# Kernel tuning notes

Measured on AMD Instinct MI355X. Metric: run time of the kernel, lower is better.

The kernel has to match this reference:

```python
import jax, jax.numpy as jnp
import numpy as np
import math

EMBED_DIM = 512
NUM_HEADS = 8
B, T = 1, 4096

def setup_inputs() -> dict:
    key = jax.random.key(0)
    ks = jax.random.split(key, 12)
    D = EMBED_DIM
    s = 1.0 / math.sqrt(D)
    inp = {
        "x": jax.random.normal(ks[0], (B, T, D), dtype=jnp.float32),
        "ln1_scale": jnp.ones((D,), jnp.float32),
        "ln1_bias": jnp.zeros((D,), jnp.float32),
        "Wq": jax.random.normal(ks[1], (D, D), jnp.float32) * s,
        "bq": jnp.zeros((D,), jnp.float32),
        "Wk": jax.random.normal(ks[2], (D, D), jnp.float32) * s,
        "bk": jnp.zeros((D,), jnp.float32),
        "Wv": jax.random.normal(ks[3], (D, D), jnp.float32) * s,
        "bv": jnp.zeros((D,), jnp.float32),
        "Wo": jax.random.normal(ks[4], (D, D), jnp.float32) * s,
        "bo": jnp.zeros((D,), jnp.float32),
        "ln2_scale": jnp.ones((D,), jnp.float32),
        "ln2_bias": jnp.zeros((D,), jnp.float32),
        "W1": jax.random.normal(ks[5], (D, 4 * D), jnp.float32) * s,
        "b1": jnp.zeros((4 * D,), jnp.float32),
        "W2": jax.random.normal(ks[6], (4 * D, D), jnp.float32) * (1.0 / math.sqrt(4 * D)),
        "b2": jnp.zeros((D,), jnp.float32),
    }
    return inp

def _layernorm(x, scale, bias, eps=1e-6):
    mu = jnp.mean(x, axis=-1, keepdims=True)
    var = jnp.mean(jnp.square(x - mu), axis=-1, keepdims=True)
    return (x - mu) * jax.lax.rsqrt(var + eps) * scale + bias

def reference(x, ln1_scale, ln1_bias, Wq, bq, Wk, bk, Wv, bv, Wo, bo,
              ln2_scale, ln2_bias, W1, b1, W2, b2):
    Bb, Tt, D = x.shape
    H = NUM_HEADS
    hd = D // H
    residual = x
    h = _layernorm(x, ln1_scale, ln1_bias)
    q = (h @ Wq + bq).reshape(Bb, Tt, H, hd).transpose(0, 2, 1, 3)
    k = (h @ Wk + bk).reshape(Bb, Tt, H, hd).transpose(0, 2, 1, 3)
    v = (h @ Wv + bv).reshape(Bb, Tt, H, hd).transpose(0, 2, 1, 3)
    # [B,H,T,T] scores (naive attention as in the original module)
    scores = jnp.einsum('bhqd,bhkd->bhqk', q, k) / math.sqrt(hd)
    probs = jax.nn.softmax(scores, axis=-1)
    out = jnp.einsum('bhqk,bhkd->bhqd', probs, v).transpose(0, 2, 1, 3).reshape(Bb, Tt, D)
    h = out @ Wo + bo  # dropout deterministic -> identity
    x = h + residual
    residual = x
    h = _layernorm(x, ln2_scale, ln2_bias)
    h = jax.nn.gelu(h @ W1 + b1, approximate=True)
    h = h @ W2 + b2
    return h + residual
```

## Files before the change

### kernel.cpp

```cpp
#include <hip/hip_runtime.h>
#include <hip/hip_bf16.h>
#include <stdint.h>

typedef __bf16 bf16;
typedef __bf16 bf16x4 __attribute__((ext_vector_type(4)));
typedef __bf16 bf16x8 __attribute__((ext_vector_type(8)));
typedef float  f32x4  __attribute__((ext_vector_type(4)));
typedef float  f32x16 __attribute__((ext_vector_type(16)));

#define MFMA32(A_, B_, C_) __builtin_amdgcn_mfma_f32_32x32x16_bf16((A_), (B_), (C_), 0, 0, 0)

#define QSCALE 0.1803368801111137f

__device__ __forceinline__ void gload_lds16(const void* g, void* l) {
  __builtin_amdgcn_global_load_lds(
      (const __attribute__((address_space(1))) unsigned int*)g,
      (__attribute__((address_space(3))) unsigned int*)l, 16, 0, 0);
}

__device__ __forceinline__ unsigned pk2(float lo, float hi_) {
  union { bf16 h[2]; unsigned u; } t;
  t.h[0] = (bf16)lo; t.h[1] = (bf16)hi_;
  return t.u;
}

__device__ __forceinline__ float fast_exp2(float x) {
#if __has_builtin(__builtin_amdgcn_exp2f)
  return __builtin_amdgcn_exp2f(x);
#else
  return exp2f(x);
#endif
}

__global__ __launch_bounds__(256) void prep_ln(const float* __restrict__ Wq,
                                               const float* __restrict__ Wk,
                                               const float* __restrict__ Wv,
                                               const float* __restrict__ Wo,
                                               const float* __restrict__ W1,
                                               const float* __restrict__ W2,
                                               const float* __restrict__ bq,
                                               const float* __restrict__ bk,
                                               const float* __restrict__ bv,
                                               bf16* __restrict__ wqkvT, bf16* __restrict__ woT,
                                               bf16* __restrict__ w1T, bf16* __restrict__ w2T,
                                               float* __restrict__ bqkv,
                                               const float* __restrict__ x,
                                               const float* __restrict__ ln1s,
                                               const float* __restrict__ ln1b,
                                               bf16* __restrict__ h) {
  const int b = blockIdx.x;
  if (b >= 774) {
    const int w = threadIdx.x >> 6, l = threadIdx.x & 63;
    const int row = (b - 774) * 4 + w;
    const float4* xp = (const float4*)(x + (size_t)row * 512 + l * 8);
    float4 v0 = xp[0], v1 = xp[1];
    float xv[8] = {v0.x, v0.y, v0.z, v0.w, v1.x, v1.y, v1.z, v1.w};
    float s = 0.f, q = 0.f;
#pragma unroll
    for (int j = 0; j < 8; ++j) { s += xv[j]; q += xv[j] * xv[j]; }
#pragma unroll
    for (int m = 1; m < 64; m <<= 1) { s += __shfl_xor(s, m); q += __shfl_xor(q, m); }
    const float mean = s * (1.f / 512.f);
    const float var = q * (1.f / 512.f) - mean * mean;
    const float rstd = rsqrtf(var + 1e-6f);
    const float4* scp = (const float4*)(ln1s + l * 8);
    const float4* bip = (const float4*)(ln1b + l * 8);
    float4 s0 = scp[0], s1 = scp[1], b0 = bip[0], b1 = bip[1];
    float sv[8] = {s0.x, s0.y, s0.z, s0.w, s1.x, s1.y, s1.z, s1.w};
    float bvv[8] = {b0.x, b0.y, b0.z, b0.w, b1.x, b1.y, b1.z, b1.w};
    bf16x8 ov;
#pragma unroll
    for (int j = 0; j < 8; ++j) ov[j] = (bf16)((xv[j] - mean) * rstd * sv[j] + bvv[j]);
    *(bf16x8*)(h + (size_t)row * 512 + l * 8) = ov;
    return;
  }
  if (b >= 768) {
    int i = (b - 768) * 256 + threadIdx.x;
    if (i < 1536)
      bqkv[i] = (i < 512) ? bq[i] * QSCALE : (i < 1024 ? bk[i - 512] : bv[i - 1024]);
    return;
  }
  const float* in; bf16* outp; int K, N, t; float sc = 1.f;
  if (b < 64)       { in = Wq; outp = wqkvT;              K = 512;  N = 512;  t = b;       sc = QSCALE; }
  else if (b < 128) { in = Wk; outp = wqkvT + 512 * 512;  K = 512;  N = 512;  t = b - 64;  }
  else if (b < 192) { in = Wv; outp = wqkvT + 1024 * 512; K = 512;  N = 512;  t = b - 128; }
  else if (b < 256) { in = Wo; outp = woT;                K = 512;  N = 512;  t = b - 192; }
  else if (b < 512) { in = W1; outp = w1T;                K = 512;  N = 2048; t = b - 256; }
  else              { in = W2; outp = w2T;                K = 2048; N = 512;  t = b - 512; }
  const int tx = K >> 6;
  const int k0 = (t % tx) * 64, n0 = (t / tx) * 64;
  __shared__ bf16 tile[64][72];
  const int tid = threadIdx.x;
#pragma unroll
  for (int s = 0; s < 16; ++s) {
    int j = tid + s * 256;
    int r = j >> 6, c = j & 63;
    tile[r][c] = (bf16)(in[(size_t)(k0 + r) * N + n0 + c] * sc);
  }
  __syncthreads();
#pragma unroll
  for (int s = 0; s < 16; ++s) {
    int j = tid + s * 256;
    int n = j >> 6, k = j & 63;
    outp[(size_t)(n0 + n) * K + k0 + k] = tile[k][n];
  }
}

__global__ __launch_bounds__(256) void ln_k(const float* __restrict__ x,
                                            const float* __restrict__ sc,
                                            const float* __restrict__ bi,
                                            bf16* __restrict__ out) {
  const int w = threadIdx.x >> 6, l = threadIdx.x & 63;
  const int row = blockIdx.x * 4 + w;
  const float4* xp = (const float4*)(x + (size_t)row * 512 + l * 8);
  float4 v0 = xp[0], v1 = xp[1];
  float xv[8] = {v0.x, v0.y, v0.z, v0.w, v1.x, v1.y, v1.z, v1.w};
  float s = 0.f, q = 0.f;
#pragma unroll
  for (int j = 0; j < 8; ++j) { s += xv[j]; q += xv[j] * xv[j]; }
#pragma unroll
  for (int m = 1; m < 64; m <<= 1) { s += __shfl_xor(s, m); q += __shfl_xor(q, m); }
  const float mean = s * (1.f / 512.f);
  const float var = q * (1.f / 512.f) - mean * mean;
  const float rstd = rsqrtf(var + 1e-6f);
  const float4* scp = (const float4*)(sc + l * 8);
  const float4* bip = (const float4*)(bi + l * 8);
  float4 s0 = scp[0], s1 = scp[1], b0 = bip[0], b1 = bip[1];
  float sv[8] = {s0.x, s0.y, s0.z, s0.w, s1.x, s1.y, s1.z, s1.w};
  float bvv[8] = {b0.x, b0.y, b0.z, b0.w, b1.x, b1.y, b1.z, b1.w};
  bf16x8 ov;
#pragma unroll
  for (int j = 0; j < 8; ++j) ov[j] = (bf16)((xv[j] - mean) * rstd * sv[j] + bvv[j]);
  *(bf16x8*)(out + (size_t)row * 512 + l * 8) = ov;
}

template <int EPI>
__global__ __launch_bounds__(256, 3) void gemm32(const bf16* __restrict__ A,
                                                 const bf16* __restrict__ Bt,
                                                 const float* __restrict__ bias,
                                                 const float* __restrict__ res,
                                                 void* __restrict__ outp,
                                                 int M, int N, int K) {
  __shared__ bf16 a_lds[3][64 * 64];
  __shared__ bf16 b_lds[3][64 * 64];
  const int m0 = blockIdx.x * 64, n0 = blockIdx.y * 64;
  const int tid = threadIdx.x, l = tid & 63, w = tid >> 6;
  const int wm = w >> 1, wn = w & 1;
  const int hi = l >> 5, l5 = l & 31;
  const int lr = l >> 3;
  const int cs = (l & 7) ^ (lr & 7);
  const int swl = l5 & 7;

  const bf16* ag = A + (size_t)(m0 + w * 16 + lr) * K + cs * 8;
  const bf16* bg = Bt + (size_t)(n0 + w * 16 + lr) * K + cs * 8;
  const size_t r8 = (size_t)8 * K;

#define GS32(B_)                                                   \
  do {                                                             \
    gload_lds16(ag,      (char*)a_lds[(B_)] + (w * 16) * 128);     \
    gload_lds16(ag + r8, (char*)a_lds[(B_)] + (w * 16 + 8) * 128); \
    gload_lds16(bg,      (char*)b_lds[(B_)] + (w * 16) * 128);     \
    gload_lds16(bg + r8, (char*)b_lds[(B_)] + (w * 16 + 8) * 128); \
    ag += 64; bg += 64;                                            \
  } while (0)

  f32x16 acc = {};
  const int kiters = K >> 6;
  GS32(0);
  GS32(1);
  asm volatile("s_waitcnt vmcnt(4)" ::: "memory");
  __builtin_amdgcn_s_barrier();
  for (int kt = 0; kt < kiters; ++kt) {
    if (kt + 2 < kiters) GS32((kt + 2) % 3);
    const bf16* ab = a_lds[kt % 3] + (wm * 32 + l5) * 64;
    const bf16* bb = b_lds[kt % 3] + (wn * 32 + l5) * 64;
#pragma unroll
    for (int kk = 0; kk < 4; ++kk) {
      bf16x8 af = *(const bf16x8*)(ab + ((kk * 2 + hi) ^ swl) * 8);
      bf16x8 bf_ = *(const bf16x8*)(bb + ((kk * 2 + hi) ^ swl) * 8);
      acc = MFMA32(bf_, af, acc);
    }
    if (kt + 1 < kiters) {
      if (kt + 2 < kiters) asm volatile("s_waitcnt vmcnt(4)" ::: "memory");
      else                 asm volatile("s_waitcnt vmcnt(0)" ::: "memory");
      __builtin_amdgcn_s_barrier();
    }
  }
#undef GS32

  const int row = m0 + wm * 32 + l5;
#pragma unroll
  for (int rg = 0; rg < 4; ++rg) {
    const int cb = n0 + wn * 32 + rg * 8 + hi * 4;
    float4 bb4 = *(const float4*)(bias + cb);
    float v[4];
    v[0] = acc[rg * 4 + 0] + bb4.x;
    v[1] = acc[rg * 4 + 1] + bb4.y;
    v[2] = acc[rg * 4 + 2] + bb4.z;
    v[3] = acc[rg * 4 + 3] + bb4.w;
    float4 rr = *(const float4*)(res + (size_t)row * N + cb);
    *(float4*)((float*)outp + (size_t)row * N + cb) =
        make_float4(v[0] + rr.x, v[1] + rr.y, v[2] + rr.z, v[3] + rr.w);
  }
}

template <int EPI>
__global__ __launch_bounds__(256, 3) void gemm_w(const bf16* __restrict__ A,
                                                 const bf16* __restrict__ Bt,
                                                 const float* __restrict__ bias,
                                                 void* __restrict__ outp,
                                                 bf16* __restrict__ k2,
                                                 bf16* __restrict__ v2,
                                                 int M, int N, int K) {
  __shared__ __align__(16) char smem[49152];
  char* a_lds = smem;
  char* b_lds = smem + 24576;
  const int tid = threadIdx.x, l = tid & 63, w = tid >> 6;
  const int wm = w >> 1, wn = w & 1;
  const int hi = l >> 5, l5 = l & 31;
  const int m0 = blockIdx.x * 128, n0 = blockIdx.y * 128;
  const int swl = l5 & 7;

  const int sr = tid >> 3, sp = tid & 7;
  const int slc = sp ^ (sr & 7);
  const int shalf = slc >> 2, skc = slc & 3;
  const bf16* ag = A + (size_t)(m0 + shalf * 64 + sr) * K + skc * 8;
  const bf16* bg = Bt + (size_t)(n0 + shalf * 64 + sr) * K + skc * 8;
  const size_t r32 = (size_t)32 * K;

#define GSW(B_)                                                       \
  do {                                                                \
    gload_lds16(ag,       a_lds + (B_) * 8192 + w * 1024);            \
    gload_lds16(ag + r32, a_lds + (B_) * 8192 + 4096 + w * 1024);     \
    gload_lds16(bg,       b_lds + (B_) * 8192 + w * 1024);            \
    gload_lds16(bg + r32, b_lds + (B_) * 8192 + 4096 + w * 1024);     \
    ag += 32; bg += 32;                                               \
  } while (0)

  f32x16 acc00 = {}, acc01 = {}, acc10 = {}, acc11 = {};
  const int kiters = K >> 5;
  GSW(0);
  GSW(1);
  asm volatile("s_waitcnt vmcnt(4)" ::: "memory");
  __builtin_amdgcn_s_barrier();
  for (int kt = 0; kt < kiters; ++kt) {
    if (kt + 2 < kiters) GSW((kt + 2) % 3);
    const char* ab = a_lds + (kt % 3) * 8192;
    const char* bb = b_lds + (kt % 3) * 8192;
#pragma unroll
    for (int kk = 0; kk < 2; ++kk) {
      bf16x8 af0 = *(const bf16x8*)(ab + (l5)*128      + ((wm * 4 + kk * 2 + hi) ^ swl) * 16);
      bf16x8 af1 = *(const bf16x8*)(ab + (32 + l5)*128 + ((wm * 4 + kk * 2 + hi) ^ swl) * 16);
      bf16x8 bf0 = *(const bf16x8*)(bb + (l5)*128      + ((wn * 4 + kk * 2 + hi) ^ swl) * 16);
      bf16x8 bf1 = *(const bf16x8*)(bb + (32 + l5)*128 + ((wn * 4 + kk * 2 + hi) ^ swl) * 16);
      acc00 = MFMA32(bf0, af0, acc00);
      acc01 = MFMA32(bf1, af0, acc01);
      acc10 = MFMA32(bf0, af1, acc10);
      acc11 = MFMA32(bf1, af1, acc11);
    }
    if (kt + 1 < kiters) {
      if (kt + 2 < kiters) asm volatile("s_waitcnt vmcnt(4)" ::: "memory");
      else                 asm volatile("s_waitcnt vmcnt(0)" ::: "memory");
      __builtin_amdgcn_s_barrier();
    }
  }
#undef GSW

  if constexpr (EPI == 2) {
#pragma unroll
    for (int mi = 0; mi < 2; ++mi) {
      const int row = m0 + wm * 64 + mi * 32 + l5;
#pragma unroll
      for (int ni = 0; ni < 2; ++ni) {
        const f32x16& ac = (mi == 0) ? (ni == 0 ? acc00 : acc01)
                                     : (ni == 0 ? acc10 : acc11);
#pragma unroll
        for (int rg = 0; rg < 4; ++rg) {
          const int cb = n0 + wn * 64 + ni * 32 + rg * 8 + hi * 4;
          float4 bb4 = *(const float4*)(bias + cb);
          float v[4] = {ac[rg * 4 + 0] + bb4.x, ac[rg * 4 + 1] + bb4.y,
                        ac[rg * 4 + 2] + bb4.z, ac[rg * 4 + 3] + bb4.w};
          bf16x4 o;
#pragma unroll
          for (int e = 0; e < 4; ++e) {
            float t = -2.3022077697f * (v[e] + 0.044715f * v[e] * v[e] * v[e]);
            o[e] = (bf16)(v[e] / (1.f + fast_exp2(t)));
          }
          *(bf16x4*)((bf16*)outp + (size_t)row * N + cb) = o;
        }
      }
    }
  } else {
    __syncthreads();
    bf16(*ct)[136] = (bf16(*)[136])smem;
#pragma unroll
    for (int mi = 0; mi < 2; ++mi) {
      const int rl = wm * 64 + mi * 32 + l5;
#pragma unroll
      for (int ni = 0; ni < 2; ++ni) {
        const f32x16& ac = (mi == 0) ? (ni == 0 ? acc00 : acc01)
                                     : (ni == 0 ? acc10 : acc11);
#pragma unroll
        for (int rg = 0; rg < 4; ++rg) {
          const int cl = wn * 64 + ni * 32 + rg * 8 + hi * 4;
          float4 bb4 = *(const float4*)(bias + n0 + cl);
          bf16x4 o;
          o[0] = (bf16)(ac[rg * 4 + 0] + bb4.x);
          o[1] = (bf16)(ac[rg * 4 + 1] + bb4.y);
          o[2] = (bf16)(ac[rg * 4 + 2] + bb4.z);
          o[3] = (bf16)(ac[rg * 4 + 3] + bb4.w);
          *(bf16x4*)(&ct[rl][cl]) = o;
        }
      }
    }
    __syncthreads();
    if (n0 < 512) {
#pragma unroll
      for (int p = 0; p < 8; ++p) {
        int v = p * 256 + tid;
        int r = v >> 4, c8 = (v & 15) * 8;
        *(bf16x8*)((bf16*)outp + (size_t)(m0 + r) * 512 + n0 + c8) =
            *(const bf16x8*)(&ct[r][c8]);
      }
    } else if (n0 < 1024) {
      const int hb = (n0 - 512) >> 6;
#pragma unroll
      for (int p = 0; p < 8; ++p) {
        int v = p * 256 + tid;
        int r = v >> 4, c8 = (v & 15) * 8;
        *(bf16x8*)(k2 + (size_t)(hb + (c8 >> 6)) * 262144 +
                   (size_t)(m0 + r) * 64 + (c8 & 63)) = *(const bf16x8*)(&ct[r][c8]);
      }
    } else {
      const int hb = (n0 - 1024) >> 6;
      const int d = tid >> 2, t8 = (tid & 3) * 8;
#pragma unroll
      for (int h2 = 0; h2 < 2; ++h2) {
        bf16* vb = v2 + (size_t)(hb + h2) * 262144 + (size_t)(m0 >> 5) * 2048;
#pragma unroll
        for (int p = 0; p < 4; ++p) {
          bf16x8 vv;
#pragma unroll
          for (int e = 0; e < 8; ++e) vv[e] = ct[p * 32 + t8 + e][h2 * 64 + d];
          *(bf16x8*)(vb + p * 2048 + d * 32 + t8) = vv;
        }
      }
    }
  }
}

__global__ __launch_bounds__(512, 4) void attn_k(const bf16* __restrict__ q2,
                                                 const bf16* __restrict__ k2,
                                                 const bf16* __restrict__ v2,
                                                 bf16* __restrict__ attnb) {
  const int bid = blockIdx.x;
  const int head = bid & 7;
  const int qt = bid >> 3;
  const int w = threadIdx.x >> 6, l = threadIdx.x & 63;
  const int hi = l >> 5, l5 = l & 31;
  const int pair = w >> 1, wq = w & 1;

  __shared__ __align__(16) char smem[65536];
  char* kt_l = smem + pair * 16384;
  char* vt_l = kt_l + 8192;

  const int qrow0 = qt * 64 + wq * 32;
  const bf16* qb = q2 + (size_t)(qrow0 + l5) * 512 + head * 64;
  bf16x8 qf[4];
#pragma unroll
  for (int cc = 0; cc < 4; ++cc) qf[cc] = *(const bf16x8*)(qb + cc * 16 + hi * 8);

  const int kstart = pair * 1024;

  const int lr = l >> 3;
  const int lc3 = (l & 7) ^ lr;
  const char* kg = (const char*)k2 + (size_t)head * 524288 + (size_t)kstart * 128 +
                   (wq * 16 + lr) * 128 + lc3 * 16;
  const char* vg = (const char*)v2 + (size_t)head * 524288 + (size_t)(kstart >> 5) * 4096 +
                   (lc3 >> 2) * 2048 + (wq * 16 + lr) * 64 + (lc3 & 3) * 16;
  const int kdst = wq * 2048;

#define STAGE(B_)                                                            \
  do {                                                                       \
    gload_lds16(kg,        kt_l + (B_) * 4096 + kdst);                       \
    gload_lds16(kg + 1024, kt_l + (B_) * 4096 + kdst + 1024);                \
    gload_lds16(vg,        vt_l + (B_) * 4096 + kdst);                       \
    gload_lds16(vg + 512,  vt_l + (B_) * 4096 + kdst + 1024);                \
    kg += 4096; vg += 4096;                                                  \
  } while (0)

  STAGE(0);
  __syncthreads();

  f32x16 o0 = {}, o1 = {};
  float psum = 0.f;
  const int swl = l5 & 7;
  const char* kbase = kt_l + l5 * 128;
  const char* vbase = vt_l + l5 * 128;

  for (int t = 0; t < 32; ++t) {
    const int cur = t & 1;
    if (t < 31) STAGE(cur ^ 1);

    __builtin_amdgcn_s_setprio(1);
    f32x16 s = {};
#pragma unroll
    for (int cc = 0; cc < 4; ++cc) {
      bf16x8 kf = *(const bf16x8*)(kbase + cur * 4096 + ((cc * 2 + hi) ^ swl) * 16);
      s = MFMA32(kf, qf[cc], s);
    }
    __builtin_amdgcn_s_setprio(0);

#pragma unroll
    for (int c = 0; c < 2; ++c) {
      float p[8];
#pragma unroll
      for (int j = 0; j < 8; ++j) p[j] = fast_exp2(s[c * 8 + j]);
      psum += ((p[0] + p[1]) + (p[2] + p[3])) + ((p[4] + p[5]) + (p[6] + p[7]));
      unsigned X = pk2(p[0], p[1]), X2 = pk2(p[2], p[3]);
      unsigned Y = pk2(p[4], p[5]), Y2 = pk2(p[6], p[7]);
      asm volatile("v_permlane32_swap_b32 %0, %1" : "+v"(X), "+v"(Y));
      asm volatile("v_permlane32_swap_b32 %0, %1" : "+v"(X2), "+v"(Y2));
      union { unsigned wd[4]; bf16x8 v; } pa;
      pa.wd[0] = X; pa.wd[1] = X2; pa.wd[2] = Y; pa.wd[3] = Y2;
      bf16x8 vf0 = *(const bf16x8*)(vbase + cur * 4096 + ((c * 2 + hi) ^ swl) * 16);
      bf16x8 vf1 = *(const bf16x8*)(vbase + cur * 4096 + ((4 + c * 2 + hi) ^ swl) * 16);
      __builtin_amdgcn_s_setprio(1);
      o0 = MFMA32(vf0, pa.v, o0);
      o1 = MFMA32(vf1, pa.v, o1);
      __builtin_amdgcn_s_setprio(0);
    }
    __syncthreads();
  }
#undef STAGE

  float* comb = (float*)smem;
  if (pair > 0) {
    float* cb = comb + (((pair - 1) * 2 + wq) * 64 + l) * 33;
#pragma unroll
    for (int r = 0; r < 16; ++r) { cb[r] = o0[r]; cb[16 + r] = o1[r]; }
    cb[32] = psum;
  }
  __syncthreads();
  if (pair == 0) {
#pragma unroll
    for (int p = 0; p < 3; ++p) {
      const float* cb = comb + ((p * 2 + wq) * 64 + l) * 33;
#pragma unroll
      for (int r = 0; r < 16; ++r) { o0[r] += cb[r]; o1[r] += cb[16 + r]; }
      psum += cb[32];
    }
    const float lsum = psum + __shfl_xor(psum, 32);
    const float inv = 1.f / lsum;
    bf16* ob = attnb + (size_t)(qrow0 + l5) * 512 + head * 64;
#pragma unroll
    for (int dt = 0; dt < 2; ++dt)
#pragma unroll
      for (int rg = 0; rg < 4; ++rg) {
        bf16x4 vv;
#pragma unroll
        for (int e = 0; e < 4; ++e) {
          const float ov = (dt == 0) ? o0[rg * 4 + e] : o1[rg * 4 + e];
          vv[e] = (bf16)(ov * inv);
        }
        *(bf16x4*)(ob + dt * 32 + rg * 8 + hi * 4) = vv;
      }
  }
}

extern "C" void kernel_launch(void* const* d_in, const int* in_sizes, int n_in,
                              void* d_out, int out_size, void* d_ws, size_t ws_size,
                              hipStream_t stream) {
  const float* x    = (const float*)d_in[0];
  const float* ln1s = (const float*)d_in[1];
  const float* ln1b = (const float*)d_in[2];
  const float* Wq   = (const float*)d_in[3];
  const float* bq   = (const float*)d_in[4];
  const float* Wk   = (const float*)d_in[5];
  const float* bk   = (const float*)d_in[6];
  const float* Wv   = (const float*)d_in[7];
  const float* bv   = (const float*)d_in[8];
  const float* Wo   = (const float*)d_in[9];
  const float* bo   = (const float*)d_in[10];
  const float* ln2s = (const float*)d_in[11];
  const float* ln2b = (const float*)d_in[12];
  const float* W1   = (const float*)d_in[13];
  const float* b1   = (const float*)d_in[14];
  const float* W2   = (const float*)d_in[15];
  const float* b2   = (const float*)d_in[16];
  float* out = (float*)d_out;

  char* ws = (char*)d_ws;
  bf16*  wqkvT = (bf16*)(ws + 0);
  bf16*  woT   = (bf16*)(ws + 1572864);
  bf16*  w1T   = (bf16*)(ws + 2097152);
  bf16*  w2T   = (bf16*)(ws + 4194304);
  float* bqkv  = (float*)(ws + 6291456);
  float* x2    = (float*)(ws + 6297600);
  bf16*  h     = (bf16*)(ws + 14686208);
  bf16*  q2    = (bf16*)(ws + 18880512);
  bf16*  k2    = (bf16*)(ws + 23074816);
  bf16*  v2    = (bf16*)(ws + 27269120);
  bf16*  attnb = h;
  bf16*  h2    = h;
  bf16*  gbuf  = (bf16*)(ws + 18880512);

  prep_ln<<<1798, 256, 0, stream>>>(Wq, Wk, Wv, Wo, W1, W2, bq, bk, bv,
                                    wqkvT, woT, w1T, w2T, bqkv, x, ln1s, ln1b, h);
  gemm_w<3><<<dim3(32, 12), 256, 0, stream>>>(h, wqkvT, bqkv, q2, k2, v2,
                                              4096, 1536, 512);
  attn_k<<<512, 512, 0, stream>>>(q2, k2, v2, attnb);
  gemm32<1><<<dim3(64, 8), 256, 0, stream>>>(attnb, woT, bo, x, x2, 4096, 512, 512);
  ln_k<<<1024, 256, 0, stream>>>(x2, ln2s, ln2b, h2);
  gemm_w<2><<<dim3(32, 16), 256, 0, stream>>>(h2, w1T, b1, gbuf, nullptr, nullptr,
                                              4096, 2048, 512);
  gemm32<1><<<dim3(64, 8), 256, 0, stream>>>(gbuf, w2T, b2, x2, out, 4096, 512, 2048);
}
```

Before: 133.0 us.

## Replace 64x64 residual GEMM with 128x64 tile, BK=32, two accumulators per wave

The two N=512 residual-add GEMMs (out-projection and FFN down-projection) now use a 128x64 output tile with K-step 32 and two MFMA accumulators per wave instead of a 64x64 tile with K-step 64. Each B fragment is reused across two A fragments, which cuts LDS traffic per MFMA and halves the grid to 256 blocks. The change also raises the occupancy hint to 4 and asks for a 2x unroll of the attention inner loop. The smaller grid may underfill the 256 CUs, and the shorter K-step doubles the number of barriers per tile.

```diff
diff --git a/kernel.cpp b/kernel.cpp
--- a/kernel.cpp
+++ b/kernel.cpp
@@ -135,72 +135,76 @@
 }
 
 template <int EPI>
-__global__ __launch_bounds__(256, 3) void gemm32(const bf16* __restrict__ A,
-                                                 const bf16* __restrict__ Bt,
-                                                 const float* __restrict__ bias,
-                                                 const float* __restrict__ res,
-                                                 void* __restrict__ outp,
-                                                 int M, int N, int K) {
-  __shared__ bf16 a_lds[3][64 * 64];
-  __shared__ bf16 b_lds[3][64 * 64];
-  const int m0 = blockIdx.x * 64, n0 = blockIdx.y * 64;
+__global__ __launch_bounds__(256, 4) void gemm_n64(const bf16* __restrict__ A,
+                                                   const bf16* __restrict__ Bt,
+                                                   const float* __restrict__ bias,
+                                                   const float* __restrict__ res,
+                                                   void* __restrict__ outp,
+                                                   int M, int N, int K) {
+  __shared__ __align__(16) char smem[36864];
   const int tid = threadIdx.x, l = tid & 63, w = tid >> 6;
   const int wm = w >> 1, wn = w & 1;
   const int hi = l >> 5, l5 = l & 31;
-  const int lr = l >> 3;
-  const int cs = (l & 7) ^ (lr & 7);
+  const int m0 = blockIdx.x * 128, n0 = blockIdx.y * 64;
   const int swl = l5 & 7;
 
-  const bf16* ag = A + (size_t)(m0 + w * 16 + lr) * K + cs * 8;
-  const bf16* bg = Bt + (size_t)(n0 + w * 16 + lr) * K + cs * 8;
-  const size_t r8 = (size_t)8 * K;
-
-#define GS32(B_)                                                   \
-  do {                                                             \
-    gload_lds16(ag,      (char*)a_lds[(B_)] + (w * 16) * 128);     \
-    gload_lds16(ag + r8, (char*)a_lds[(B_)] + (w * 16 + 8) * 128); \
-    gload_lds16(bg,      (char*)b_lds[(B_)] + (w * 16) * 128);     \
-    gload_lds16(bg + r8, (char*)b_lds[(B_)] + (w * 16 + 8) * 128); \
-    ag += 64; bg += 64;                                            \
+  const int sr = tid >> 3, sp = tid & 7;
+  const int slc = sp ^ (sr & 7);
+  const int shalf = slc >> 2, skc = slc & 3;
+  const bf16* ag = A + (size_t)(m0 + shalf * 64 + sr) * K + skc * 8;
+  const size_t r32 = (size_t)32 * K;
+  const int brow = tid >> 3;
+  const int blc = sp ^ (brow & 7);
+  const bf16* bg = Bt + (size_t)(n0 + (blc >> 2) * 32 + brow) * K + (blc & 3) * 8;
+
+#define GSN(B_)                                                          \
+  do {                                                                   \
+    char* ab_ = smem + (B_) * 12288;                                     \
+    gload_lds16(ag,       ab_ + w * 1024);                               \
+    gload_lds16(ag + r32, ab_ + 4096 + w * 1024);                        \
+    gload_lds16(bg,       ab_ + 8192 + w * 1024);                        \
+    ag += 32; bg += 32;                                                  \
   } while (0)
 
-  f32x16 acc = {};
-  const int kiters = K >> 6;
-  GS32(0);
-  GS32(1);
-  asm volatile("s_waitcnt vmcnt(4)" ::: "memory");
+  f32x16 acc0 = {}, acc1 = {};
+  const int kiters = K >> 5;
+  GSN(0);
+  GSN(1);
+  asm volatile("s_waitcnt vmcnt(3)" ::: "memory");
   __builtin_amdgcn_s_barrier();
   for (int kt = 0; kt < kiters; ++kt) {
-    if (kt + 2 < kiters) GS32((kt + 2) % 3);
-    const bf16* ab = a_lds[kt % 3] + (wm * 32 + l5) * 64;
-    const bf16* bb = b_lds[kt % 3] + (wn * 32 + l5) * 64;
-#pragma unroll
-    for (int kk = 0; kk < 4; ++kk) {
-      bf16x8 af = *(const bf16x8*)(ab + ((kk * 2 + hi) ^ swl) * 8);
-      bf16x8 bf_ = *(const bf16x8*)(bb + ((kk * 2 + hi) ^ swl) * 8);
-      acc = MFMA32(bf_, af, acc);
+    if (kt + 2 < kiters) GSN((kt + 2) % 3);
+    const char* ab = smem + (kt % 3) * 12288;
+    const char* bb = ab + 8192;
+#pragma unroll
+    for (int kk = 0; kk < 2; ++kk) {
+      bf16x8 af0 = *(const bf16x8*)(ab + (l5)*128      + ((wm * 4 + kk * 2 + hi) ^ swl) * 16);
+      bf16x8 af1 = *(const bf16x8*)(ab + (32 + l5)*128 + ((wm * 4 + kk * 2 + hi) ^ swl) * 16);
+      bf16x8 bf_ = *(const bf16x8*)(bb + (l5)*128      + ((wn * 4 + kk * 2 + hi) ^ swl) * 16);
+      acc0 = MFMA32(bf_, af0, acc0);
+      acc1 = MFMA32(bf_, af1, acc1);
     }
     if (kt + 1 < kiters) {
-      if (kt + 2 < kiters) asm volatile("s_waitcnt vmcnt(4)" ::: "memory");
+      if (kt + 2 < kiters) asm volatile("s_waitcnt vmcnt(3)" ::: "memory");
       else                 asm volatile("s_waitcnt vmcnt(0)" ::: "memory");
       __builtin_amdgcn_s_barrier();
     }
   }
-#undef GS32
-
-  const int row = m0 + wm * 32 + l5;
-#pragma unroll
-  for (int rg = 0; rg < 4; ++rg) {
-    const int cb = n0 + wn * 32 + rg * 8 + hi * 4;
-    float4 bb4 = *(const float4*)(bias + cb);
-    float v[4];
-    v[0] = acc[rg * 4 + 0] + bb4.x;
-    v[1] = acc[rg * 4 + 1] + bb4.y;
-    v[2] = acc[rg * 4 + 2] + bb4.z;
-    v[3] = acc[rg * 4 + 3] + bb4.w;
-    float4 rr = *(const float4*)(res + (size_t)row * N + cb);
-    *(float4*)((float*)outp + (size_t)row * N + cb) =
-        make_float4(v[0] + rr.x, v[1] + rr.y, v[2] + rr.z, v[3] + rr.w);
+#undef GSN
+
+#pragma unroll
+  for (int mi = 0; mi < 2; ++mi) {
+    const int row = m0 + wm * 64 + mi * 32 + l5;
+    const f32x16& ac = (mi == 0) ? acc0 : acc1;
+#pragma unroll
+    for (int rg = 0; rg < 4; ++rg) {
+      const int cb = n0 + wn * 32 + rg * 8 + hi * 4;
+      float4 bb4 = *(const float4*)(bias + cb);
+      float4 rr = *(const float4*)(res + (size_t)row * N + cb);
+      *(float4*)((float*)outp + (size_t)row * N + cb) =
+          make_float4(ac[rg * 4 + 0] + bb4.x + rr.x, ac[rg * 4 + 1] + bb4.y + rr.y,
+                      ac[rg * 4 + 2] + bb4.z + rr.z, ac[rg * 4 + 3] + bb4.w + rr.w);
+    }
   }
 }
 
@@ -398,6 +402,7 @@
   const char* kbase = kt_l + l5 * 128;
   const char* vbase = vt_l + l5 * 128;
 
+#pragma unroll 2
   for (int t = 0; t < 32; ++t) {
     const int cur = t & 1;
     if (t < 31) STAGE(cur ^ 1);
@@ -510,9 +515,9 @@
   gemm_w<3><<<dim3(32, 12), 256, 0, stream>>>(h, wqkvT, bqkv, q2, k2, v2,
                                               4096, 1536, 512);
   attn_k<<<512, 512, 0, stream>>>(q2, k2, v2, attnb);
-  gemm32<1><<<dim3(64, 8), 256, 0, stream>>>(attnb, woT, bo, x, x2, 4096, 512, 512);
+  gemm_n64<1><<<dim3(32, 8), 256, 0, stream>>>(attnb, woT, bo, x, x2, 4096, 512, 512);
   ln_k<<<1024, 256, 0, stream>>>(x2, ln2s, ln2b, h2);
   gemm_w<2><<<dim3(32, 16), 256, 0, stream>>>(h2, w1T, b1, gbuf, nullptr, nullptr,
                                               4096, 2048, 512);
-  gemm32<1><<<dim3(64, 8), 256, 0, stream>>>(gbuf, w2T, b2, x2, out, 4096, 512, 2048);
-}
+  gemm_n64<1><<<dim3(32, 8), 256, 0, stream>>>(gbuf, w2T, b2, x2, out, 4096, 512, 2048);
+}
```

Result: no change. 131.1 us (-1.4%).
